# Kernel tuning notes

Measured on AMD Instinct MI355X. Metric: run time of the kernel, lower is better.

The kernel has to match this reference:

```python
import jax, jax.numpy as jnp
import numpy as np

B, S, D, H = 2, 2048, 1024, 16
DK = D // H


def setup_inputs() -> dict:
    key = jax.random.key(0)
    ks = jax.random.split(key, 12)
    scale = 1.0 / np.sqrt(D)
    inp = {
        "Q": jax.random.normal(ks[0], (B, S, D), jnp.float32),
        "K": jax.random.normal(ks[1], (B, S, D), jnp.float32),
        "V": jax.random.normal(ks[2], (B, S, D), jnp.float32),
        # causal mask, broadcast over batch: [B, S, S]
        "mask": jnp.broadcast_to(jnp.tril(jnp.ones((S, S), jnp.bool_)), (B, S, S)),
        "WQ_w": jax.random.normal(ks[3], (D, D), jnp.float32) * scale,
        "WQ_b": jnp.zeros((D,), jnp.float32),
        "WK_w": jax.random.normal(ks[4], (D, D), jnp.float32) * scale,
        "WK_b": jnp.zeros((D,), jnp.float32),
        "WV_w": jax.random.normal(ks[5], (D, D), jnp.float32) * scale,
        "WV_b": jnp.zeros((D,), jnp.float32),
        "WO_w": jax.random.normal(ks[6], (D, D), jnp.float32) * scale,
        "WO_b": jnp.zeros((D,), jnp.float32),
    }
    return inp


def reference(Q, K, V, mask, WQ_w, WQ_b, WK_w, WK_b, WV_w, WV_b, WO_w, WO_b):
    # Linear projections (torch Linear: x @ W.T + b), split heads -> [B,H,S,DK]
    def proj(x, w, b):
        return (x @ w.T + b).reshape(B, S, H, DK).transpose(0, 2, 1, 3)

    q = proj(Q, WQ_w, WQ_b)
    k = proj(K, WK_w, WK_b)
    v = proj(V, WV_w, WV_b)

    scores = jnp.einsum("bhqd,bhkd->bhqk", q, k) / jnp.sqrt(jnp.asarray(DK, q.dtype))
    scores = jnp.where(mask[:, None, :, :], scores, -jnp.inf)
    attn = jax.nn.softmax(scores, axis=-1)  # dropout is identity in eval mode

    out = jnp.einsum("bhqk,bhkd->bhqd", attn, v)
    out = out.transpose(0, 2, 1, 3).reshape(B, S, D)
    out = out @ WO_w.T + WO_b
    return (out, attn)
```

## Files before the change

kernel.cpp:

```cpp
#include <hip/hip_runtime.h>

#define S_LEN 2048
#define DMODEL 1024
#define NHEAD 16
#define DKH 64
#define BATCH 2

typedef __bf16 bf16_t;
typedef __bf16 bf16x8 __attribute__((ext_vector_type(8)));
typedef __bf16 bf16x4 __attribute__((ext_vector_type(4)));
typedef float f32x4 __attribute__((ext_vector_type(4)));

__device__ __forceinline__ void gload16(const bf16_t* g, bf16_t* l) {
  __builtin_amdgcn_global_load_lds(
      (const __attribute__((address_space(1))) unsigned int*)g,
      (__attribute__((address_space(3))) unsigned int*)l,
      16, 0, 0);
}

__global__ void cvt_all(const float* __restrict__ Q, const float* __restrict__ K,
                        const float* __restrict__ V, const float* __restrict__ WQ,
                        const float* __restrict__ WK, const float* __restrict__ WV,
                        const float* __restrict__ WO, bf16_t* __restrict__ dst) {
  const int i = blockIdx.x * 256 + threadIdx.x;
  const float* src;
  int off;
  if (i < 1572864) {
    const int seg = i >> 19;
    off = i & 524287;
    src = (seg == 0) ? Q : ((seg == 1) ? K : V);
  } else {
    const int j = i - 1572864;
    const int seg = j >> 17;
    off = j & 131071;
    src = (seg == 0) ? WQ : ((seg == 1) ? WK : ((seg == 2) ? WV : WO));
  }
  f32x4 a = *(const f32x4*)(src + (size_t)off * 8);
  f32x4 b = *(const f32x4*)(src + (size_t)off * 8 + 4);
  bf16x8 v;
#pragma unroll
  for (int j = 0; j < 4; ++j) { v[j] = (bf16_t)a[j]; v[4 + j] = (bf16_t)b[j]; }
  *(bf16x8*)(dst + (size_t)i * 8) = v;
}

struct GOp {
  const bf16_t* A;
  const bf16_t* W;
  const float* bias;
  char* out;
  int emode;
};

#define GM 4096
#define GN 1024
#define GK 1024
#define BM 128
#define BN 128
#define BK 64

__launch_bounds__(256, 3)
__global__ void gemm_bf16(GOp op0, GOp op1, GOp op2) {
  GOp op = (blockIdx.z == 0) ? op0 : ((blockIdx.z == 1) ? op1 : op2);
  const int n0 = blockIdx.x * BN;
  const int m0 = blockIdx.y * BM;
  const int t = threadIdx.x;
  const int w = t >> 6;
  const int l = t & 63;
  const int wr = w >> 1, wc = w & 1;
  const int lg = l >> 4, ll = l & 15;
  const int sr = l >> 3;
  const int sc = l & 7;

  __shared__ __align__(16) bf16_t Asm[BM * BK];
  __shared__ __align__(16) bf16_t Bsm[BM * BK];

  f32x4 acc[4][4] = {};

  for (int kt = 0; kt < GK / BK; ++kt) {
    __syncthreads();
#pragma unroll
    for (int i = 0; i < 4; ++i) {
      const int rbase = i * 32 + (w << 3);
      const int row = rbase + sr;
      const int gc = (sc ^ (row & 7)) << 3;
      gload16(op.A + (size_t)(m0 + row) * GK + kt * BK + gc, &Asm[rbase * BK]);
      gload16(op.W + (size_t)(n0 + row) * GK + kt * BK + gc, &Bsm[rbase * BK]);
    }
    __syncthreads();

    bf16x8 af[4][2], bfr[4][2];
#pragma unroll
    for (int mi = 0; mi < 4; ++mi) {
      const int row = wr * 64 + mi * 16 + ll;
      af[mi][0] = *(const bf16x8*)&Asm[row * BK + ((lg ^ (row & 7)) << 3)];
      af[mi][1] = *(const bf16x8*)&Asm[row * BK + (((4 + lg) ^ (row & 7)) << 3)];
    }
#pragma unroll
    for (int ni = 0; ni < 4; ++ni) {
      const int row = wc * 64 + ni * 16 + ll;
      bfr[ni][0] = *(const bf16x8*)&Bsm[row * BK + ((lg ^ (row & 7)) << 3)];
      bfr[ni][1] = *(const bf16x8*)&Bsm[row * BK + (((4 + lg) ^ (row & 7)) << 3)];
    }
#pragma unroll
    for (int mi = 0; mi < 4; ++mi)
#pragma unroll
      for (int ni = 0; ni < 4; ++ni) {
        acc[mi][ni] = __builtin_amdgcn_mfma_f32_16x16x32_bf16(af[mi][0], bfr[ni][0], acc[mi][ni], 0, 0, 0);
        acc[mi][ni] = __builtin_amdgcn_mfma_f32_16x16x32_bf16(af[mi][1], bfr[ni][1], acc[mi][ni], 0, 0, 0);
      }
  }

#pragma unroll
  for (int mi = 0; mi < 4; ++mi) {
#pragma unroll
    for (int ni = 0; ni < 4; ++ni) {
      const int col = n0 + wc * 64 + ni * 16 + ll;
      const int rbase = m0 + wr * 64 + mi * 16 + (lg << 2);
      const float bval = op.bias[col];
      f32x4 v = acc[mi][ni];
      if (op.emode == 0) {
        bf16_t* o = (bf16_t*)op.out;
#pragma unroll
        for (int r = 0; r < 4; ++r)
          o[(size_t)(rbase + r) * GN + col] = (bf16_t)(v[r] + bval);
      } else {
        const int hh = col >> 6, dd = col & 63;
        const int bb = rbase >> 11, ss = rbase & (S_LEN - 1);
        bf16_t* o = (bf16_t*)op.out + (((size_t)bb * NHEAD + hh) * DKH + dd) * S_LEN + ss;
        bf16x4 pk;
#pragma unroll
        for (int r = 0; r < 4; ++r) pk[r] = (bf16_t)(v[r] + bval);
        *(bf16x4*)o = pk;
      }
    }
  }
}

__launch_bounds__(256, 4)
__global__ void gemm_out64(const bf16_t* __restrict__ A, const bf16_t* __restrict__ W,
                           const float* __restrict__ bias, float* __restrict__ out) {
  const int n0 = blockIdx.x * 128;
  const int m0 = blockIdx.y * 64;
  const int t = threadIdx.x;
  const int w = t >> 6;
  const int l = t & 63;
  const int wr = w >> 1, wc = w & 1;
  const int lg = l >> 4, ll = l & 15;
  const int sr = l >> 3;
  const int sc = l & 7;

  __shared__ __align__(16) bf16_t Asm[64 * BK];
  __shared__ __align__(16) bf16_t Bsm[128 * BK];

  f32x4 acc[2][4] = {};

  for (int kt = 0; kt < GK / BK; ++kt) {
    __syncthreads();
    {
#pragma unroll
      for (int i = 0; i < 2; ++i) {
        const int rbase = i * 32 + (w << 3);
        const int row = rbase + sr;
        const int gc = (sc ^ (row & 7)) << 3;
        gload16(A + (size_t)(m0 + row) * GK + kt * BK + gc, &Asm[rbase * BK]);
      }
#pragma unroll
      for (int i = 0; i < 4; ++i) {
        const int rbase = i * 32 + (w << 3);
        const int row = rbase + sr;
        const int gc = (sc ^ (row & 7)) << 3;
        gload16(W + (size_t)(n0 + row) * GK + kt * BK + gc, &Bsm[rbase * BK]);
      }
    }
    __syncthreads();

    bf16x8 af[2][2], bfr[4][2];
#pragma unroll
    for (int mi = 0; mi < 2; ++mi) {
      const int row = wr * 32 + mi * 16 + ll;
      af[mi][0] = *(const bf16x8*)&Asm[row * BK + ((lg ^ (row & 7)) << 3)];
      af[mi][1] = *(const bf16x8*)&Asm[row * BK + (((4 + lg) ^ (row & 7)) << 3)];
    }
#pragma unroll
    for (int ni = 0; ni < 4; ++ni) {
      const int row = wc * 64 + ni * 16 + ll;
      bfr[ni][0] = *(const bf16x8*)&Bsm[row * BK + ((lg ^ (row & 7)) << 3)];
      bfr[ni][1] = *(const bf16x8*)&Bsm[row * BK + (((4 + lg) ^ (row & 7)) << 3)];
    }
#pragma unroll
    for (int mi = 0; mi < 2; ++mi)
#pragma unroll
      for (int ni = 0; ni < 4; ++ni) {
        acc[mi][ni] = __builtin_amdgcn_mfma_f32_16x16x32_bf16(af[mi][0], bfr[ni][0], acc[mi][ni], 0, 0, 0);
        acc[mi][ni] = __builtin_amdgcn_mfma_f32_16x16x32_bf16(af[mi][1], bfr[ni][1], acc[mi][ni], 0, 0, 0);
      }
  }

#pragma unroll
  for (int mi = 0; mi < 2; ++mi) {
#pragma unroll
    for (int ni = 0; ni < 4; ++ni) {
      const int col = n0 + wc * 64 + ni * 16 + ll;
      const int rbase = m0 + wr * 32 + mi * 16 + (lg << 2);
      const float bval = bias[col];
      f32x4 v = acc[mi][ni];
#pragma unroll
      for (int r = 0; r < 4; ++r)
        out[(size_t)(rbase + r) * GN + col] = v[r] + bval;
    }
  }
}

__launch_bounds__(256, 2)
__global__ void attn2(const bf16_t* __restrict__ qp, const bf16_t* __restrict__ kp,
                      const bf16_t* __restrict__ vT, float* __restrict__ attn_out,
                      bf16_t* __restrict__ ctx) {
  const int raw = blockIdx.x;
  const int wg = (raw & 7) * 64 + (raw >> 3);
  const int bh = wg >> 4;
  const int pr = wg & 15;
  const int b = bh >> 4, h = bh & 15;
  const int flip = (raw >> 8) & 1;

  __shared__ __align__(16) bf16_t Qs[64 * 64];
  __shared__ __align__(16) bf16_t Ks[2][128 * 64];
  __shared__ __align__(16) bf16_t Vs[2][2][64 * 64];
  __shared__ __align__(16) bf16_t Pt[4][16 * 64];
  float* rinvS = (float*)&Pt[0][0];

  const int t = threadIdx.x;
  const int w = t >> 6;
  const int l = t & 63;
  const int lg = l >> 4;
  const int ll = l & 15;
  const int sr = l >> 3;
  const int sc = l & 7;

  const bf16_t* kbh = kp + (size_t)b * S_LEN * DMODEL + h * DKH;
  const bf16_t* vbh = vT + (size_t)bh * DKH * S_LEN;

#define KV_STAGE128(bu, ktt)                                                              \
  {                                                                                       \
    _Pragma("unroll") for (int i = 0; i < 4; ++i) {                                       \
      const int rbase = i * 32 + (w << 3);                                                \
      const int row = rbase + sr;                                                         \
      const int gc = (sc ^ (row & 7)) << 3;                                               \
      gload16(kbh + (size_t)((ktt) * 128 + row) * DMODEL + gc, &Ks[bu][rbase * 64]);      \
    }                                                                                     \
    _Pragma("unroll") for (int i = 0; i < 2; ++i) {                                       \
      const int rbase = i * 32 + (w << 3);                                                \
      const int row = rbase + sr;                                                         \
      const int gc = (sc ^ (row & 7)) << 3;                                               \
      gload16(vbh + (size_t)row * S_LEN + (ktt) * 128 + gc, &Vs[bu][0][rbase * 64]);      \
      gload16(vbh + (size_t)row * S_LEN + (ktt) * 128 + 64 + gc, &Vs[bu][1][rbase * 64]); \
    }                                                                                     \
  }

#define K_STAGE(bu, kt)                                                            \
  {                                                                                \
    _Pragma("unroll") for (int i = 0; i < 2; ++i) {                                \
      const int rbase = i * 32 + (w << 3);                                         \
      const int row = rbase + sr;                                                  \
      const int gc = (sc ^ (row & 7)) << 3;                                        \
      gload16(kbh + (size_t)((kt) * 64 + row) * DMODEL + gc, &Ks[bu][rbase * 64]); \
    }                                                                              \
  }

  for (int half = 0; half < 2; ++half) {
    const int qt = (half ^ flip) ? (31 - pr) : pr;
    const int q0 = qt * 64;
    const int nktt = (qt + 2) >> 1;

    __syncthreads();
#pragma unroll
    for (int i = 0; i < 2; ++i) {
      const int rbase = i * 32 + (w << 3);
      const int row = rbase + sr;
      const int gc = (sc ^ (row & 7)) << 3;
      gload16(qp + (size_t)(b * S_LEN + q0 + row) * DMODEL + h * DKH + gc, &Qs[rbase * 64]);
    }
    KV_STAGE128(0, 0);
    __syncthreads();

    bf16x8 qf0, qf1;
    {
      const int row = w * 16 + ll;
      qf0 = *(const bf16x8*)&Qs[row * 64 + ((lg ^ (row & 7)) << 3)];
      qf1 = *(const bf16x8*)&Qs[row * 64 + (((4 + lg) ^ (row & 7)) << 3)];
    }

    f32x4 oacc[4] = {};
    float sums[4] = {0.f, 0.f, 0.f, 0.f};
    const int qrow_base = q0 + w * 16 + (lg << 2);

    int cur = 0;
    for (int ktt = 0; ktt < nktt; ++ktt) {
      if (ktt + 1 < nktt) KV_STAGE128(cur ^ 1, ktt + 1);

      __builtin_amdgcn_s_setprio(1);
#pragma unroll
      for (int s = 0; s < 2; ++s) {
        const int kk = 2 * ktt + s;
        if (kk <= qt) {
          const bool diag = (kk == qt);
#pragma unroll
          for (int cb = 0; cb < 4; ++cb) {
            const int lr = s * 64 + cb * 16 + ll;
            bf16x8 kf0 = *(const bf16x8*)&Ks[cur][lr * 64 + ((lg ^ (lr & 7)) << 3)];
            bf16x8 kf1 = *(const bf16x8*)&Ks[cur][lr * 64 + (((4 + lg) ^ (lr & 7)) << 3)];
            f32x4 a = {0.f, 0.f, 0.f, 0.f};
            a = __builtin_amdgcn_mfma_f32_16x16x32_bf16(qf0, kf0, a, 0, 0, 0);
            a = __builtin_amdgcn_mfma_f32_16x16x32_bf16(qf1, kf1, a, 0, 0, 0);
            const int gcol = kk * 64 + cb * 16 + ll;
            if (diag) {
#pragma unroll
              for (int r = 0; r < 4; ++r) {
                const float e = (gcol <= qrow_base + r) ? __expf(a[r] * 0.125f) : 0.0f;
                sums[r] += e;
                const int ql = (lg << 2) + r;
                const int k = cb * 16 + ll;
                *(bf16_t*)((char*)&Pt[w][0] + ql * 128 + (((k >> 3) ^ (ql & 7)) << 4) + ((k & 7) << 1)) = (bf16_t)e;
              }
            } else {
#pragma unroll
              for (int r = 0; r < 4; ++r) {
                const float e = __expf(a[r] * 0.125f);
                sums[r] += e;
                const int ql = (lg << 2) + r;
                const int k = cb * 16 + ll;
                *(bf16_t*)((char*)&Pt[w][0] + ql * 128 + (((k >> 3) ^ (ql & 7)) << 4) + ((k & 7) << 1)) = (bf16_t)e;
              }
            }
          }
          bf16x8 pa0 = *(const bf16x8*)((char*)&Pt[w][0] + ll * 128 + ((lg ^ (ll & 7)) << 4));
          bf16x8 pa1 = *(const bf16x8*)((char*)&Pt[w][0] + ll * 128 + (((4 + lg) ^ (ll & 7)) << 4));
#pragma unroll
          for (int db = 0; db < 4; ++db) {
            const int drow = db * 16 + ll;
            bf16x8 vf0 = *(const bf16x8*)&Vs[cur][s][drow * 64 + ((lg ^ (drow & 7)) << 3)];
            bf16x8 vf1 = *(const bf16x8*)&Vs[cur][s][drow * 64 + (((4 + lg) ^ (drow & 7)) << 3)];
            oacc[db] = __builtin_amdgcn_mfma_f32_16x16x32_bf16(pa0, vf0, oacc[db], 0, 0, 0);
            oacc[db] = __builtin_amdgcn_mfma_f32_16x16x32_bf16(pa1, vf1, oacc[db], 0, 0, 0);
          }
        }
      }
      __builtin_amdgcn_s_setprio(0);
      __syncthreads();
      cur ^= 1;
    }

    float rinv[4];
#pragma unroll
    for (int r = 0; r < 4; ++r) {
      float s = sums[r];
      s += __shfl_xor(s, 1);
      s += __shfl_xor(s, 2);
      s += __shfl_xor(s, 4);
      s += __shfl_xor(s, 8);
      rinv[r] = 1.0f / s;
    }
    if (ll == 0) {
#pragma unroll
      for (int r = 0; r < 4; ++r) rinvS[w * 16 + (lg << 2) + r] = rinv[r];
    }

    K_STAGE(0, 0);

#pragma unroll
    for (int db = 0; db < 4; ++db)
#pragma unroll
      for (int r = 0; r < 4; ++r) {
        const int grow = q0 + w * 16 + (lg << 2) + r;
        ctx[(size_t)(b * S_LEN + grow) * DMODEL + h * DKH + db * 16 + ll] = (bf16_t)(oacc[db][r] * rinv[r]);
      }
    __syncthreads();

    const float rv = rinvS[w * 16 + ll];
    float* arow = attn_out + ((size_t)bh * S_LEN + q0) * S_LEN;

    for (int kt = qt + 1; kt < 32; ++kt) {
      f32x4 z = {0.f, 0.f, 0.f, 0.f};
#pragma unroll
      for (int j = 0; j < 4; ++j) {
        const int row = w * 16 + (lg << 2) + j;
        *(f32x4*)(arow + (size_t)row * S_LEN + kt * 64 + (ll << 2)) = z;
      }
    }

    const int qrow_sw = q0 + w * 16 + ll;
    int cur2 = 0;
    for (int kt = 0; kt <= qt; ++kt) {
      if (kt + 1 <= qt) K_STAGE(cur2 ^ 1, kt + 1);

      const bool diag = (kt == qt);
#pragma unroll
      for (int i = 0; i < 4; ++i) {
        const int krow = i * 16 + ll;
        bf16x8 kf0 = *(const bf16x8*)&Ks[cur2][krow * 64 + ((lg ^ (krow & 7)) << 3)];
        bf16x8 kf1 = *(const bf16x8*)&Ks[cur2][krow * 64 + (((4 + lg) ^ (krow & 7)) << 3)];
        f32x4 a = {0.f, 0.f, 0.f, 0.f};
        a = __builtin_amdgcn_mfma_f32_16x16x32_bf16(kf0, qf0, a, 0, 0, 0);
        a = __builtin_amdgcn_mfma_f32_16x16x32_bf16(kf1, qf1, a, 0, 0, 0);
        const int kbase = kt * 64 + i * 16 + (lg << 2);
        f32x4 o;
        if (diag) {
#pragma unroll
          for (int r = 0; r < 4; ++r)
            o[r] = (kbase + r <= qrow_sw) ? __expf(a[r] * 0.125f) * rv : 0.0f;
        } else {
#pragma unroll
          for (int r = 0; r < 4; ++r) o[r] = __expf(a[r] * 0.125f) * rv;
        }
        *(f32x4*)(arow + (size_t)(w * 16 + ll) * S_LEN + kbase) = o;
      }
      __syncthreads();
      cur2 ^= 1;
    }
  }
#undef KV_STAGE128
#undef K_STAGE
}

extern "C" void kernel_launch(void* const* d_in, const int* in_sizes, int n_in,
                              void* d_out, int out_size, void* d_ws, size_t ws_size,
                              hipStream_t stream) {
  const float* Q   = (const float*)d_in[0];
  const float* K   = (const float*)d_in[1];
  const float* V   = (const float*)d_in[2];
  const float* WQw = (const float*)d_in[4];
  const float* WQb = (const float*)d_in[5];
  const float* WKw = (const float*)d_in[6];
  const float* WKb = (const float*)d_in[7];
  const float* WVw = (const float*)d_in[8];
  const float* WVb = (const float*)d_in[9];
  const float* WOw = (const float*)d_in[10];
  const float* WOb = (const float*)d_in[11];

  char* ws = (char*)d_ws;
  bf16_t* qb  = (bf16_t*)(ws);
  bf16_t* kb  = (bf16_t*)(ws + (size_t)( 8 << 20));
  bf16_t* vb  = (bf16_t*)(ws + (size_t)(16 << 20));
  bf16_t* wq  = (bf16_t*)(ws + (size_t)(24 << 20));
  bf16_t* wk  = (bf16_t*)(ws + (size_t)(26 << 20));
  bf16_t* wv  = (bf16_t*)(ws + (size_t)(28 << 20));
  bf16_t* wo  = (bf16_t*)(ws + (size_t)(30 << 20));
  bf16_t* qp  = (bf16_t*)(ws + (size_t)(32 << 20));
  bf16_t* kp  = (bf16_t*)(ws + (size_t)(40 << 20));
  bf16_t* vT  = (bf16_t*)(ws + (size_t)(48 << 20));
  bf16_t* ctx = (bf16_t*)(ws + (size_t)(56 << 20));

  float* out_main = (float*)d_out;
  float* attn_out = out_main + (size_t)BATCH * S_LEN * DMODEL;

  cvt_all<<<dim3(8192), 256, 0, stream>>>(Q, K, V, WQw, WKw, WVw, WOw, (bf16_t*)ws);

  GOp opq{qb, wq, WQb, (char*)qp, 0};
  GOp opk{kb, wk, WKb, (char*)kp, 0};
  GOp opv{vb, wv, WVb, (char*)vT, 1};
  gemm_bf16<<<dim3(8, 32, 3), 256, 0, stream>>>(opq, opk, opv);

  attn2<<<dim3(512), 256, 0, stream>>>(qp, kp, vT, attn_out, ctx);

  gemm_out64<<<dim3(8, 64), 256, 0, stream>>>(ctx, wo, WOb, out_main);
}
```

Measured before the change: 213.8 us.

## Use 128-row query tiles per block with zigzag causal scheduling in attention

```diff
diff --git a/kernel.cpp b/kernel.cpp
--- a/kernel.cpp
+++ b/kernel.cpp
@@ -156,21 +156,19 @@
 
   for (int kt = 0; kt < GK / BK; ++kt) {
     __syncthreads();
-    {
-#pragma unroll
-      for (int i = 0; i < 2; ++i) {
-        const int rbase = i * 32 + (w << 3);
-        const int row = rbase + sr;
-        const int gc = (sc ^ (row & 7)) << 3;
-        gload16(A + (size_t)(m0 + row) * GK + kt * BK + gc, &Asm[rbase * BK]);
-      }
-#pragma unroll
-      for (int i = 0; i < 4; ++i) {
-        const int rbase = i * 32 + (w << 3);
-        const int row = rbase + sr;
-        const int gc = (sc ^ (row & 7)) << 3;
-        gload16(W + (size_t)(n0 + row) * GK + kt * BK + gc, &Bsm[rbase * BK]);
-      }
+#pragma unroll
+    for (int i = 0; i < 2; ++i) {
+      const int rbase = i * 32 + (w << 3);
+      const int row = rbase + sr;
+      const int gc = (sc ^ (row & 7)) << 3;
+      gload16(A + (size_t)(m0 + row) * GK + kt * BK + gc, &Asm[rbase * BK]);
+    }
+#pragma unroll
+    for (int i = 0; i < 4; ++i) {
+      const int rbase = i * 32 + (w << 3);
+      const int row = rbase + sr;
+      const int gc = (sc ^ (row & 7)) << 3;
+      gload16(W + (size_t)(n0 + row) * GK + kt * BK + gc, &Bsm[rbase * BK]);
     }
     __syncthreads();
 
@@ -212,21 +210,26 @@
 }
 
 __launch_bounds__(256, 2)
-__global__ void attn2(const bf16_t* __restrict__ qp, const bf16_t* __restrict__ kp,
+__global__ void attn5(const bf16_t* __restrict__ qp, const bf16_t* __restrict__ kp,
                       const bf16_t* __restrict__ vT, float* __restrict__ attn_out,
                       bf16_t* __restrict__ ctx) {
   const int raw = blockIdx.x;
   const int wg = (raw & 7) * 64 + (raw >> 3);
   const int bh = wg >> 4;
-  const int pr = wg & 15;
+  const int i4 = wg & 15;
+  const int zig = (i4 & 1) ? (15 - (i4 >> 1)) : (i4 >> 1);
+  const int qt = (bh & 2) ? (15 - zig) : zig;
   const int b = bh >> 4, h = bh & 15;
-  const int flip = (raw >> 8) & 1;
-
-  __shared__ __align__(16) bf16_t Qs[64 * 64];
-  __shared__ __align__(16) bf16_t Ks[2][128 * 64];
-  __shared__ __align__(16) bf16_t Vs[2][2][64 * 64];
-  __shared__ __align__(16) bf16_t Pt[4][16 * 64];
-  float* rinvS = (float*)&Pt[0][0];
+  const int q0 = qt * 128;
+  const int nkt = 2 * qt + 2;
+
+  __shared__ __align__(16) bf16_t SMEM[32768];
+  bf16_t* Qs  = SMEM;
+  bf16_t* KsB = SMEM + 8192;
+  bf16_t* VsB = SMEM + 16384;
+  bf16_t* PtB = SMEM + 24576;
+  bf16_t* KB  = SMEM;
+  float* rinvS = (float*)PtB;
 
   const int t = threadIdx.x;
   const int w = t >> 6;
@@ -235,190 +238,210 @@
   const int ll = l & 15;
   const int sr = l >> 3;
   const int sc = l & 7;
+  char* PtW = (char*)PtB + (w << 12);
 
   const bf16_t* kbh = kp + (size_t)b * S_LEN * DMODEL + h * DKH;
   const bf16_t* vbh = vT + (size_t)bh * DKH * S_LEN;
 
-#define KV_STAGE128(bu, ktt)                                                              \
+#define KV_STAGE(bu, kt_)                                                                 \
   {                                                                                       \
-    _Pragma("unroll") for (int i = 0; i < 4; ++i) {                                       \
-      const int rbase = i * 32 + (w << 3);                                                \
-      const int row = rbase + sr;                                                         \
-      const int gc = (sc ^ (row & 7)) << 3;                                               \
-      gload16(kbh + (size_t)((ktt) * 128 + row) * DMODEL + gc, &Ks[bu][rbase * 64]);      \
-    }                                                                                     \
     _Pragma("unroll") for (int i = 0; i < 2; ++i) {                                       \
       const int rbase = i * 32 + (w << 3);                                                \
       const int row = rbase + sr;                                                         \
       const int gc = (sc ^ (row & 7)) << 3;                                               \
-      gload16(vbh + (size_t)row * S_LEN + (ktt) * 128 + gc, &Vs[bu][0][rbase * 64]);      \
-      gload16(vbh + (size_t)row * S_LEN + (ktt) * 128 + 64 + gc, &Vs[bu][1][rbase * 64]); \
+      gload16(kbh + (size_t)((kt_) * 64 + row) * DMODEL + gc, KsB + (bu) * 4096 + rbase * 64); \
+      gload16(vbh + (size_t)row * S_LEN + (kt_) * 64 + gc, VsB + (bu) * 4096 + rbase * 64);    \
     }                                                                                     \
   }
 
-#define K_STAGE(bu, kt)                                                            \
-  {                                                                                \
-    _Pragma("unroll") for (int i = 0; i < 2; ++i) {                                \
-      const int rbase = i * 32 + (w << 3);                                         \
-      const int row = rbase + sr;                                                  \
-      const int gc = (sc ^ (row & 7)) << 3;                                        \
-      gload16(kbh + (size_t)((kt) * 64 + row) * DMODEL + gc, &Ks[bu][rbase * 64]); \
-    }                                                                              \
-  }
-
-  for (int half = 0; half < 2; ++half) {
-    const int qt = (half ^ flip) ? (31 - pr) : pr;
-    const int q0 = qt * 64;
-    const int nktt = (qt + 2) >> 1;
-
-    __syncthreads();
-#pragma unroll
-    for (int i = 0; i < 2; ++i) {
-      const int rbase = i * 32 + (w << 3);
-      const int row = rbase + sr;
-      const int gc = (sc ^ (row & 7)) << 3;
-      gload16(qp + (size_t)(b * S_LEN + q0 + row) * DMODEL + h * DKH + gc, &Qs[rbase * 64]);
-    }
-    KV_STAGE128(0, 0);
-    __syncthreads();
-
-    bf16x8 qf0, qf1;
-    {
-      const int row = w * 16 + ll;
-      qf0 = *(const bf16x8*)&Qs[row * 64 + ((lg ^ (row & 7)) << 3)];
-      qf1 = *(const bf16x8*)&Qs[row * 64 + (((4 + lg) ^ (row & 7)) << 3)];
-    }
-
-    f32x4 oacc[4] = {};
-    float sums[4] = {0.f, 0.f, 0.f, 0.f};
-    const int qrow_base = q0 + w * 16 + (lg << 2);
-
-    int cur = 0;
-    for (int ktt = 0; ktt < nktt; ++ktt) {
-      if (ktt + 1 < nktt) KV_STAGE128(cur ^ 1, ktt + 1);
-
-      __builtin_amdgcn_s_setprio(1);
-#pragma unroll
-      for (int s = 0; s < 2; ++s) {
-        const int kk = 2 * ktt + s;
-        if (kk <= qt) {
-          const bool diag = (kk == qt);
-#pragma unroll
-          for (int cb = 0; cb < 4; ++cb) {
-            const int lr = s * 64 + cb * 16 + ll;
-            bf16x8 kf0 = *(const bf16x8*)&Ks[cur][lr * 64 + ((lg ^ (lr & 7)) << 3)];
-            bf16x8 kf1 = *(const bf16x8*)&Ks[cur][lr * 64 + (((4 + lg) ^ (lr & 7)) << 3)];
-            f32x4 a = {0.f, 0.f, 0.f, 0.f};
-            a = __builtin_amdgcn_mfma_f32_16x16x32_bf16(qf0, kf0, a, 0, 0, 0);
-            a = __builtin_amdgcn_mfma_f32_16x16x32_bf16(qf1, kf1, a, 0, 0, 0);
-            const int gcol = kk * 64 + cb * 16 + ll;
-            if (diag) {
-#pragma unroll
-              for (int r = 0; r < 4; ++r) {
-                const float e = (gcol <= qrow_base + r) ? __expf(a[r] * 0.125f) : 0.0f;
-                sums[r] += e;
-                const int ql = (lg << 2) + r;
-                const int k = cb * 16 + ll;
-                *(bf16_t*)((char*)&Pt[w][0] + ql * 128 + (((k >> 3) ^ (ql & 7)) << 4) + ((k & 7) << 1)) = (bf16_t)e;
-              }
-            } else {
-#pragma unroll
-              for (int r = 0; r < 4; ++r) {
-                const float e = __expf(a[r] * 0.125f);
-                sums[r] += e;
-                const int ql = (lg << 2) + r;
-                const int k = cb * 16 + ll;
-                *(bf16_t*)((char*)&Pt[w][0] + ql * 128 + (((k >> 3) ^ (ql & 7)) << 4) + ((k & 7) << 1)) = (bf16_t)e;
-              }
+#define K_STAGE_KB(idx, kt_)                                                              \
+  {                                                                                       \
+    _Pragma("unroll") for (int i = 0; i < 2; ++i) {                                       \
+      const int rbase = i * 32 + (w << 3);                                                \
+      const int row = rbase + sr;                                                         \
+      const int gc = (sc ^ (row & 7)) << 3;                                               \
+      gload16(kbh + (size_t)((kt_) * 64 + row) * DMODEL + gc, KB + (idx) * 4096 + rbase * 64); \
+    }                                                                                     \
+  }
+
+#pragma unroll
+  for (int i = 0; i < 4; ++i) {
+    const int rbase = i * 32 + (w << 3);
+    const int row = rbase + sr;
+    const int gc = (sc ^ (row & 7)) << 3;
+    gload16(qp + (size_t)(b * S_LEN + q0 + row) * DMODEL + h * DKH + gc, Qs + rbase * 64);
+  }
+  KV_STAGE(0, 0);
+  __syncthreads();
+
+  bf16x8 qf[2][2];
+#pragma unroll
+  for (int s2 = 0; s2 < 2; ++s2) {
+    const int row = s2 * 64 + w * 16 + ll;
+    qf[s2][0] = *(const bf16x8*)&Qs[row * 64 + ((lg ^ (row & 7)) << 3)];
+    qf[s2][1] = *(const bf16x8*)&Qs[row * 64 + (((4 + lg) ^ (row & 7)) << 3)];
+  }
+
+  f32x4 oacc[2][4] = {};
+  float sums[2][4] = {};
+
+  int cur = 0;
+  for (int kt = 0; kt < nkt; ++kt) {
+    if (kt + 1 < nkt) KV_STAGE(cur ^ 1, kt + 1);
+
+    __builtin_amdgcn_s_setprio(1);
+#pragma unroll
+    for (int s2 = 0; s2 < 2; ++s2) {
+      const int dmax = 2 * qt + s2;
+      if (kt <= dmax) {
+        const bool diag = (kt == dmax);
+        const int qrow_base = q0 + s2 * 64 + w * 16 + (lg << 2);
+        char* PtS = PtW + (s2 << 11);
+#pragma unroll
+        for (int cb = 0; cb < 4; ++cb) {
+          const int krow = cb * 16 + ll;
+          bf16x8 kf0 = *(const bf16x8*)&KsB[cur * 4096 + krow * 64 + ((lg ^ (krow & 7)) << 3)];
+          bf16x8 kf1 = *(const bf16x8*)&KsB[cur * 4096 + krow * 64 + (((4 + lg) ^ (krow & 7)) << 3)];
+          f32x4 a = {0.f, 0.f, 0.f, 0.f};
+          a = __builtin_amdgcn_mfma_f32_16x16x32_bf16(qf[s2][0], kf0, a, 0, 0, 0);
+          a = __builtin_amdgcn_mfma_f32_16x16x32_bf16(qf[s2][1], kf1, a, 0, 0, 0);
+          const int gcol = kt * 64 + krow;
+          if (diag) {
+#pragma unroll
+            for (int r = 0; r < 4; ++r) {
+              const float e = (gcol <= qrow_base + r) ? __expf(a[r] * 0.125f) : 0.0f;
+              sums[s2][r] += e;
+              const int ql = (lg << 2) + r;
+              const int k = cb * 16 + ll;
+              *(bf16_t*)(PtS + ql * 128 + (((k >> 3) ^ (ql & 7)) << 4) + ((k & 7) << 1)) = (bf16_t)e;
+            }
+          } else {
+#pragma unroll
+            for (int r = 0; r < 4; ++r) {
+              const float e = __expf(a[r] * 0.125f);
+              sums[s2][r] += e;
+              const int ql = (lg << 2) + r;
+              const int k = cb * 16 + ll;
+              *(bf16_t*)(PtS + ql * 128 + (((k >> 3) ^ (ql & 7)) << 4) + ((k & 7) << 1)) = (bf16_t)e;
             }
           }
-          bf16x8 pa0 = *(const bf16x8*)((char*)&Pt[w][0] + ll * 128 + ((lg ^ (ll & 7)) << 4));
-          bf16x8 pa1 = *(const bf16x8*)((char*)&Pt[w][0] + ll * 128 + (((4 + lg) ^ (ll & 7)) << 4));
-#pragma unroll
-          for (int db = 0; db < 4; ++db) {
-            const int drow = db * 16 + ll;
-            bf16x8 vf0 = *(const bf16x8*)&Vs[cur][s][drow * 64 + ((lg ^ (drow & 7)) << 3)];
-            bf16x8 vf1 = *(const bf16x8*)&Vs[cur][s][drow * 64 + (((4 + lg) ^ (drow & 7)) << 3)];
-            oacc[db] = __builtin_amdgcn_mfma_f32_16x16x32_bf16(pa0, vf0, oacc[db], 0, 0, 0);
-            oacc[db] = __builtin_amdgcn_mfma_f32_16x16x32_bf16(pa1, vf1, oacc[db], 0, 0, 0);
-          }
         }
-      }
-      __builtin_amdgcn_s_setprio(0);
-      __syncthreads();
-      cur ^= 1;
-    }
-
-    float rinv[4];
+        bf16x8 pa0 = *(const bf16x8*)(PtS + ll * 128 + ((lg ^ (ll & 7)) << 4));
+        bf16x8 pa1 = *(const bf16x8*)(PtS + ll * 128 + (((4 + lg) ^ (ll & 7)) << 4));
+#pragma unroll
+        for (int db = 0; db < 4; ++db) {
+          const int drow = db * 16 + ll;
+          bf16x8 vf0 = *(const bf16x8*)&VsB[cur * 4096 + drow * 64 + ((lg ^ (drow & 7)) << 3)];
+          bf16x8 vf1 = *(const bf16x8*)&VsB[cur * 4096 + drow * 64 + (((4 + lg) ^ (drow & 7)) << 3)];
+          oacc[s2][db] = __builtin_amdgcn_mfma_f32_16x16x32_bf16(pa0, vf0, oacc[s2][db], 0, 0, 0);
+          oacc[s2][db] = __builtin_amdgcn_mfma_f32_16x16x32_bf16(pa1, vf1, oacc[s2][db], 0, 0, 0);
+        }
+      }
+    }
+    __builtin_amdgcn_s_setprio(0);
+    __syncthreads();
+    cur ^= 1;
+  }
+
+  float rinv[2][4];
+#pragma unroll
+  for (int s2 = 0; s2 < 2; ++s2)
 #pragma unroll
     for (int r = 0; r < 4; ++r) {
-      float s = sums[r];
+      float s = sums[s2][r];
       s += __shfl_xor(s, 1);
       s += __shfl_xor(s, 2);
       s += __shfl_xor(s, 4);
       s += __shfl_xor(s, 8);
-      rinv[r] = 1.0f / s;
-    }
-    if (ll == 0) {
-#pragma unroll
-      for (int r = 0; r < 4; ++r) rinvS[w * 16 + (lg << 2) + r] = rinv[r];
-    }
-
-    K_STAGE(0, 0);
-
+      rinv[s2][r] = 1.0f / s;
+    }
+  if (ll == 0) {
+#pragma unroll
+    for (int s2 = 0; s2 < 2; ++s2)
+#pragma unroll
+      for (int r = 0; r < 4; ++r)
+        rinvS[s2 * 64 + w * 16 + (lg << 2) + r] = rinv[s2][r];
+  }
+
+#pragma unroll
+  for (int j = 0; j < 3; ++j)
+    if (j < nkt) K_STAGE_KB(j, j);
+
+#pragma unroll
+  for (int s2 = 0; s2 < 2; ++s2)
 #pragma unroll
     for (int db = 0; db < 4; ++db)
 #pragma unroll
       for (int r = 0; r < 4; ++r) {
-        const int grow = q0 + w * 16 + (lg << 2) + r;
-        ctx[(size_t)(b * S_LEN + grow) * DMODEL + h * DKH + db * 16 + ll] = (bf16_t)(oacc[db][r] * rinv[r]);
-      }
-    __syncthreads();
-
-    const float rv = rinvS[w * 16 + ll];
-    float* arow = attn_out + ((size_t)bh * S_LEN + q0) * S_LEN;
-
-    for (int kt = qt + 1; kt < 32; ++kt) {
-      f32x4 z = {0.f, 0.f, 0.f, 0.f};
-#pragma unroll
-      for (int j = 0; j < 4; ++j) {
-        const int row = w * 16 + (lg << 2) + j;
-        *(f32x4*)(arow + (size_t)row * S_LEN + kt * 64 + (ll << 2)) = z;
-      }
-    }
-
-    const int qrow_sw = q0 + w * 16 + ll;
-    int cur2 = 0;
-    for (int kt = 0; kt <= qt; ++kt) {
-      if (kt + 1 <= qt) K_STAGE(cur2 ^ 1, kt + 1);
-
-      const bool diag = (kt == qt);
-#pragma unroll
-      for (int i = 0; i < 4; ++i) {
-        const int krow = i * 16 + ll;
-        bf16x8 kf0 = *(const bf16x8*)&Ks[cur2][krow * 64 + ((lg ^ (krow & 7)) << 3)];
-        bf16x8 kf1 = *(const bf16x8*)&Ks[cur2][krow * 64 + (((4 + lg) ^ (krow & 7)) << 3)];
-        f32x4 a = {0.f, 0.f, 0.f, 0.f};
-        a = __builtin_amdgcn_mfma_f32_16x16x32_bf16(kf0, qf0, a, 0, 0, 0);
-        a = __builtin_amdgcn_mfma_f32_16x16x32_bf16(kf1, qf1, a, 0, 0, 0);
-        const int kbase = kt * 64 + i * 16 + (lg << 2);
-        f32x4 o;
-        if (diag) {
-#pragma unroll
-          for (int r = 0; r < 4; ++r)
-            o[r] = (kbase + r <= qrow_sw) ? __expf(a[r] * 0.125f) * rv : 0.0f;
-        } else {
-#pragma unroll
-          for (int r = 0; r < 4; ++r) o[r] = __expf(a[r] * 0.125f) * rv;
+        const int grow = q0 + s2 * 64 + w * 16 + (lg << 2) + r;
+        ctx[(size_t)(b * S_LEN + grow) * DMODEL + h * DKH + db * 16 + ll] =
+            (bf16_t)(oacc[s2][db][r] * rinv[s2][r]);
+      }
+  __syncthreads();
+
+  float rv[2];
+  rv[0] = rinvS[w * 16 + ll];
+  rv[1] = rinvS[64 + w * 16 + ll];
+  float* arow = attn_out + ((size_t)bh * S_LEN + q0) * S_LEN;
+  const f32x4 zero4 = {0.f, 0.f, 0.f, 0.f};
+
+  {
+    const int ktz = 2 * qt + 1;
+    for (int rr = t >> 4; rr < 64; rr += 16)
+      *(f32x4*)(arow + (size_t)rr * S_LEN + ktz * 64 + ((t & 15) << 2)) = zero4;
+  }
+  for (int ktz = 2 * qt + 2; ktz < 32; ++ktz)
+    for (int rr = t >> 4; rr < 128; rr += 16)
+      *(f32x4*)(arow + (size_t)rr * S_LEN + ktz * 64 + ((t & 15) << 2)) = zero4;
+
+  const int ngrp = (nkt + 2) / 3;
+  for (int g = 0; g < ngrp; ++g) {
+    const int nb = ((g + 1) & 1) * 3;
+#pragma unroll
+    for (int j = 0; j < 3; ++j) {
+      const int kt2 = (g + 1) * 3 + j;
+      if (kt2 < nkt) K_STAGE_KB(nb + j, kt2);
+    }
+    const int cb2 = (g & 1) * 3;
+#pragma unroll
+    for (int j = 0; j < 3; ++j) {
+      const int kt = g * 3 + j;
+      if (kt < nkt) {
+        const bf16_t* Kbuf = KB + (cb2 + j) * 4096;
+#pragma unroll
+        for (int s2 = 0; s2 < 2; ++s2) {
+          const int dmax = 2 * qt + s2;
+          if (kt <= dmax) {
+            const bool diag = (kt == dmax);
+            const int qrow_sw = q0 + s2 * 64 + w * 16 + ll;
+#pragma unroll
+            for (int i = 0; i < 4; ++i) {
+              const int krow = i * 16 + ll;
+              bf16x8 kf0 = *(const bf16x8*)&Kbuf[krow * 64 + ((lg ^ (krow & 7)) << 3)];
+              bf16x8 kf1 = *(const bf16x8*)&Kbuf[krow * 64 + (((4 + lg) ^ (krow & 7)) << 3)];
+              f32x4 a = {0.f, 0.f, 0.f, 0.f};
+              a = __builtin_amdgcn_mfma_f32_16x16x32_bf16(kf0, qf[s2][0], a, 0, 0, 0);
+              a = __builtin_amdgcn_mfma_f32_16x16x32_bf16(kf1, qf[s2][1], a, 0, 0, 0);
+              const int kbase = kt * 64 + i * 16 + (lg << 2);
+              f32x4 o;
+              if (diag) {
+#pragma unroll
+                for (int r = 0; r < 4; ++r)
+                  o[r] = (kbase + r <= qrow_sw) ? __expf(a[r] * 0.125f) * rv[s2] : 0.0f;
+              } else {
+#pragma unroll
+                for (int r = 0; r < 4; ++r) o[r] = __expf(a[r] * 0.125f) * rv[s2];
+              }
+              *(f32x4*)(arow + (size_t)(s2 * 64 + w * 16 + ll) * S_LEN + kbase) = o;
+            }
+          }
         }
-        *(f32x4*)(arow + (size_t)(w * 16 + ll) * S_LEN + kbase) = o;
-      }
-      __syncthreads();
-      cur2 ^= 1;
-    }
-  }
-#undef KV_STAGE128
-#undef K_STAGE
+      }
+    }
+    __syncthreads();
+  }
+#undef KV_STAGE
+#undef K_STAGE_KB
 }
 
 extern "C" void kernel_launch(void* const* d_in, const int* in_sizes, int n_in,
@@ -459,7 +482,7 @@
   GOp opv{vb, wv, WVb, (char*)vT, 1};
   gemm_bf16<<<dim3(8, 32, 3), 256, 0, stream>>>(opq, opk, opv);
 
-  attn2<<<dim3(512), 256, 0, stream>>>(qp, kp, vT, attn_out, ctx);
+  attn5<<<dim3(512), 256, 0, stream>>>(qp, kp, vT, attn_out, ctx);
 
   gemm_out64<<<dim3(8, 64), 256, 0, stream>>>(ctx, wo, WOb, out_main);
 }
```

Measured after the change: 226.0 us. 5.7% more time.
